# Performance work log

Measured on AMD Instinct MI355X. Metric: run time of the kernel, lower is better.

## Reference

```python
import jax, jax.numpy as jnp
import numpy as np

NF = 32      # feature channels
DG = 4       # deformable groups
K = 9        # 3x3 kernel taps


def _conv(x, w, b, stride=1):
    # x: [B,C,H,W], w: [O,I,3,3] (pad=1)
    y = jax.lax.conv_general_dilated(x, w, (stride, stride), ((1, 1), (1, 1)),
                                     dimension_numbers=('NCHW', 'OIHW', 'NCHW'))
    return y + b[None, :, None, None]


def _lrelu(x):
    return jnp.where(x >= 0, x, 0.1 * x)


def _up2(x):
    # bilinear, align_corners=False (half-pixel centers, matches torch F.interpolate)
    B, C, H, W = x.shape
    return jax.image.resize(x, (B, C, 2 * H, 2 * W), method='bilinear')


def _deform_conv(x, om, w, b):
    # Modulated deformable conv (DCNv2), stride=1, pad=1, dilation=1, 3x3.
    # x: [B,C,H,W]; om: [B,3*DG*K,H,W] = (offset_y | offset_x | mask) blocks.
    B, C, H, W = x.shape
    Cg = C // DG
    o1, o2, m = jnp.split(om, 3, axis=1)
    off_y = o1.reshape(B, DG, K, H, W)
    off_x = o2.reshape(B, DG, K, H, W)
    mask = jax.nn.sigmoid(m).reshape(B, DG, K, H, W)
    k = jnp.arange(K)
    dy = (k // 3 - 1).astype(x.dtype)            # kernel tap y displacement
    dx = (k % 3 - 1).astype(x.dtype)
    # sampling positions [B,DG,K,H,W]
    py = off_y + jnp.arange(H, dtype=x.dtype)[:, None] + dy[:, None, None]
    px = off_x + jnp.arange(W, dtype=x.dtype)[None, :] + dx[:, None, None]
    y0 = jnp.floor(py)
    x0 = jnp.floor(px)
    wy1 = py - y0
    wx1 = px - x0
    y0i = y0.astype(jnp.int32)
    x0i = x0.astype(jnp.int32)
    imgf = x.reshape(B, DG, Cg, H * W)

    def corner(yi, xi, wt):
        valid = (yi >= 0) & (yi < H) & (xi >= 0) & (xi < W)
        yc = jnp.clip(yi, 0, H - 1)
        xc = jnp.clip(xi, 0, W - 1)
        idx = (yc * W + xc).reshape(B, DG, 1, K * H * W)
        v = jnp.take_along_axis(imgf, idx, axis=3).reshape(B, DG, Cg, K, H, W)
        return v * (wt * valid)[:, :, None]

    samp = (corner(y0i, x0i, (1 - wy1) * (1 - wx1))
            + corner(y0i, x0i + 1, (1 - wy1) * wx1)
            + corner(y0i + 1, x0i, wy1 * (1 - wx1))
            + corner(y0i + 1, x0i + 1, wy1 * wx1))
    samp = samp * mask[:, :, None]                       # [B,DG,Cg,K,H,W]
    out = jnp.einsum('bgckhw,ogck->bohw', samp, w.reshape(w.shape[0], DG, Cg, K))
    return out + b[None, :, None, None]


_PARAM_SHAPES = [
    ('w1_1', (32, 64, 3, 3)), ('b1_1', (32,)),
    ('w2_1', (32, 32, 3, 3)), ('b2_1', (32,)),
    ('w3_1', (32, 32, 3, 3)), ('b3_1', (32,)),
    ('w4_1', (32, 32, 3, 3)), ('b4_1', (32,)),
    ('w6_1', (32, 32, 3, 3)), ('b6_1', (32,)),
    ('w7_1', (32, 32, 3, 3)), ('b7_1', (32,)),
    ('w1_2', (32, 64, 3, 3)), ('b1_2', (32,)),
    ('w2_2', (32, 32, 3, 3)), ('b2_2', (32,)),
    ('w3_2', (32, 64, 3, 3)), ('b3_2', (32,)),
    ('w4_2', (32, 32, 3, 3)), ('b4_2', (32,)),
    ('w_om', (108, 32, 3, 3)), ('b_om', (108,)),   # DCN_sep conv_offset_mask: 3*DG*K=108
    ('w_dcn', (32, 32, 3, 3)), ('b_dcn', (32,)),
]


def setup_inputs() -> dict:
    key = jax.random.key(0)
    ks = jax.random.split(key, len(_PARAM_SHAPES) + 2)
    B, H, W = 4, 192, 192
    d = {
        'fea1': jax.random.normal(ks[0], (B, NF, H, W), jnp.float32),
        'fea2': jax.random.normal(ks[1], (B, NF, H, W), jnp.float32),
    }
    for i, (name, shp) in enumerate(_PARAM_SHAPES):
        d[name] = jax.random.normal(ks[i + 2], shp, jnp.float32) * 0.05
    return d


def reference(fea1, fea2, w1_1, b1_1, w2_1, b2_1, w3_1, b3_1, w4_1, b4_1,
              w6_1, b6_1, w7_1, b7_1, w1_2, b1_2, w2_2, b2_2, w3_2, b3_2,
              w4_2, b4_2, w_om, b_om, w_dcn, b_dcn):
    off = _lrelu(_conv(jnp.concatenate([fea1, fea2], 1), w1_1, b1_1))
    off1 = _lrelu(_conv(off, w2_1, b2_1))
    off2 = _lrelu(_conv(off1, w3_1, b3_1, 2))   # H/2
    off2 = _lrelu(_conv(off2, w4_1, b4_1))
    off3 = _lrelu(_conv(off2, w6_1, b6_1, 2))   # H/4
    off3 = _lrelu(_conv(off3, w7_1, b7_1))
    up = _up2(off3)                              # back to H/2
    off = _lrelu(_conv(jnp.concatenate([up, off2], 1), w1_2, b1_2))
    off = _lrelu(_conv(off, w2_2, b2_2))
    up = _up2(off)                               # back to H
    off = _lrelu(_conv(jnp.concatenate([up, off1], 1), w3_2, b3_2))
    base_offset = _conv(off, w4_2, b4_2)
    om = _conv(base_offset, w_om, b_om)          # DCN_sep offset/mask head
    return _deform_conv(fea2, om, w_dcn, b_dcn)
```

## Files before the change

kernel.cpp:

```cpp
#include <hip/hip_runtime.h>
#include <math.h>


#define BDIM 256

typedef __attribute__((ext_vector_type(8))) short short8v;
typedef __attribute__((ext_vector_type(4))) float f32x4;

__device__ __forceinline__ unsigned short f2bf(float f) {
    unsigned u = __builtin_bit_cast(unsigned, f);
    u = (u + 0x7FFF + ((u >> 16) & 1)) >> 16;
    return (unsigned short)u;
}
__device__ __forceinline__ float bf2f(unsigned short h) {
    unsigned u = ((unsigned)h) << 16;
    return __builtin_bit_cast(float, u);
}

template<int NPASS, int NHALF, int NT, int STRIDE, bool LRELU>
__global__ __launch_bounds__(BDIM, 2)
void convm_k(const short* __restrict__ in0, const short* __restrict__ in1,
             const short* __restrict__ wf,
             const float* __restrict__ bias,
             short* __restrict__ out,
             int Hin, int Win, int Hout, int Wout, int OCS, int coutTot)
{
    const int lane = threadIdx.x & 63;
    const int wid  = blockIdx.x * 4 + (threadIdx.x >> 6);
    const int segs = Wout / (16 * NT);
    const int b  = wid / (Hout * segs);
    int r = wid - b * (Hout * segs);
    const int oy = r / segs;
    const int x0 = (r - oy * segs) * (16 * NT);
    const int lp = lane & 15;
    const int g  = lane >> 4;

    f32x4 acc[NT][NHALF];
#pragma unroll
    for (int nt = 0; nt < NT; ++nt)
#pragma unroll
        for (int h = 0; h < NHALF; ++h)
            acc[nt][h] = (f32x4){0.f, 0.f, 0.f, 0.f};

    const size_t inPlane = (size_t)Hin * Win * 32;
    const short8v zero = {};
    constexpr bool CACHE_A = (NHALF <= 2) && (NT > 1);

#pragma unroll
    for (int pass = 0; pass < NPASS; ++pass) {
        const short* inp = (pass == 0 ? in0 : in1) + (size_t)b * inPlane;

        short8v awc[CACHE_A ? 9 * NHALF : 1];
        if constexpr (CACHE_A) {
#pragma unroll
            for (int t = 0; t < 9; ++t)
#pragma unroll
                for (int h = 0; h < NHALF; ++h)
                    awc[t * NHALF + h] = *(const short8v*)(
                        wf + ((((size_t)pass * 9 + t) * NHALF + h) * 64 + lane) * 8);
        }

#pragma unroll
        for (int t = 0; t < 9; ++t) {
            const int iy = oy * STRIDE + t / 3 - 1;
            const bool rowok = (unsigned)iy < (unsigned)Hin;
            const int iyc = min(max(iy, 0), Hin - 1);

            short8v bvs[NT];
#pragma unroll
            for (int nt = 0; nt < NT; ++nt) {
                const int ox = x0 + nt * 16 + lp;
                const int ix = ox * STRIDE + t % 3 - 1;
                const bool ok = rowok & ((unsigned)ix < (unsigned)Win);
                const int ixc = min(max(ix, 0), Win - 1);
                short8v bv = *(const short8v*)(inp + ((size_t)iyc * Win + ixc) * 32 + g * 8);
                bvs[nt] = ok ? bv : zero;
            }
#pragma unroll
            for (int h = 0; h < NHALF; ++h) {
                short8v av;
                if constexpr (CACHE_A)
                    av = awc[t * NHALF + h];
                else
                    av = *(const short8v*)(
                        wf + ((((size_t)pass * 9 + t) * NHALF + h) * 64 + lane) * 8);
#pragma unroll
                for (int nt = 0; nt < NT; ++nt)
                    acc[nt][h] = __builtin_amdgcn_mfma_f32_16x16x32_bf16(
                        av, bvs[nt], acc[nt][h], 0, 0, 0);
            }
        }
    }

    const size_t outBase = ((size_t)b * Hout + oy) * Wout;
#pragma unroll
    for (int nt = 0; nt < NT; ++nt) {
        const int p = x0 + nt * 16 + lp;
        short* op = out + (outBase + p) * OCS;
#pragma unroll
        for (int h = 0; h < NHALF; ++h) {
            ushort4 st;
#pragma unroll
            for (int j = 0; j < 4; ++j) {
                const int co = h * 16 + g * 4 + j;
                float v = acc[nt][h][j] + bias[min(co, coutTot - 1)];
                if (LRELU) v = (v >= 0.f) ? v : 0.1f * v;
                ((unsigned short*)&st)[j] = f2bf(v);
            }
            const int co0 = h * 16 + g * 4;
            if (co0 < coutTot)
                *(ushort4*)(op + co0) = st;
        }
    }
}

struct WPArgs {
    const float* src[11];
    int off[11];
    int npass[11], nhalf[11], O[11];
};

__global__ __launch_bounds__(BDIM)
void wprep_k(WPArgs a, short* __restrict__ wbase)
{
    const int z = blockIdx.z;
    const int n = a.npass[z] * 9 * a.nhalf[z] * 512;
    const int idx = blockIdx.x * BDIM + threadIdx.x;
    if (idx >= n) return;
    const int j = idx & 7;
    const int l = (idx >> 3) & 63;
    int r = idx >> 9;
    const int h = r % a.nhalf[z]; r /= a.nhalf[z];
    const int t = r % 9;
    const int pass = r / 9;
    const int I = a.npass[z] * 32;
    const int cout = h * 16 + (l & 15);
    const int cin  = pass * 32 + (l >> 4) * 8 + j;
    float v = (cout < a.O[z]) ? a.src[z][((size_t)cout * I + cin) * 9 + t] : 0.f;
    wbase[a.off[z] + idx] = (short)f2bf(v);
}

__global__ __launch_bounds__(BDIM)
void wdp_k(const float* __restrict__ w, short* __restrict__ dst)
{
    const int idx = blockIdx.x * BDIM + threadIdx.x;
    if (idx >= 9 * 2 * 64 * 8) return;
    const int j = idx & 7;
    const int l = (idx >> 3) & 63;
    const int h = (idx >> 9) & 1;
    const int k = idx >> 10;
    const int cout = h * 16 + (l & 15);
    const int cin  = (l >> 4) * 8 + j;
    dst[idx] = (short)f2bf(w[((size_t)cout * 32 + cin) * 9 + k]);
}

__global__ __launch_bounds__(BDIM)
void cvtnhwc_k(const float* __restrict__ s0, const float* __restrict__ s1,
               short* __restrict__ d0, short* __restrict__ d1, int H, int W)
{
    const float* s = blockIdx.z ? s1 : s0;
    short* d = blockIdx.z ? d1 : d0;
    const int idx = blockIdx.x * BDIM + threadIdx.x;
    if (idx >= 4 * 32 * H * W) return;
    const int c = idx & 31;
    int t = idx >> 5;
    const int x = t % W; t /= W;
    const int y = t % H;
    const int b = t / H;
    d[idx] = (short)f2bf(s[(((size_t)b * 32 + c) * H + y) * W + x]);
}

__global__ __launch_bounds__(BDIM)
void up2b_k(const short* __restrict__ in, short* __restrict__ out,
            int Hin, int Win)
{
    const int Hout = 2 * Hin, Wout = 2 * Win;
    const int idx = blockIdx.x * BDIM + threadIdx.x;
    if (idx >= 4 * Hout * Wout * 4) return;
    const int cg = idx & 3;
    int t = idx >> 2;
    const int x = t % Wout; t /= Wout;
    const int y = t % Hout;
    const int b = t / Hout;

    const float sy = (y + 0.5f) * 0.5f - 0.5f;
    const float sx = (x + 0.5f) * 0.5f - 0.5f;
    const float y0f = floorf(sy), x0f = floorf(sx);
    const float wy = sy - y0f, wx = sx - x0f;
    const int y0 = (int)y0f, x0 = (int)x0f;
    const int y0c = min(max(y0, 0), Hin - 1);
    const int y1c = min(max(y0 + 1, 0), Hin - 1);
    const int x0c = min(max(x0, 0), Win - 1);
    const int x1c = min(max(x0 + 1, 0), Win - 1);

    const short* base = in + (size_t)b * Hin * Win * 32 + cg * 8;
    short8v v00 = *(const short8v*)(base + ((size_t)y0c * Win + x0c) * 32);
    short8v v01 = *(const short8v*)(base + ((size_t)y0c * Win + x1c) * 32);
    short8v v10 = *(const short8v*)(base + ((size_t)y1c * Win + x0c) * 32);
    short8v v11 = *(const short8v*)(base + ((size_t)y1c * Win + x1c) * 32);

    short8v o;
#pragma unroll
    for (int j = 0; j < 8; ++j) {
        float f = (1.f - wy) * ((1.f - wx) * bf2f((unsigned short)v00[j]) +
                                wx * bf2f((unsigned short)v01[j]))
                + wy * ((1.f - wx) * bf2f((unsigned short)v10[j]) +
                        wx * bf2f((unsigned short)v11[j]));
        o[j] = (short)f2bf(f);
    }
    short* op = out + (size_t)b * Hout * Wout * 32 + ((size_t)y * Wout + x) * 32 + cg * 8;
    *(short8v*)op = o;
}

__global__ __launch_bounds__(BDIM, 4)
void dcnm_k(const short* __restrict__ xb,
            const short* __restrict__ om,
            const short* __restrict__ wf,
            const float* __restrict__ bias,
            float* __restrict__ out, int H, int W)
{
    const int lane = threadIdx.x & 63;
    const int wid  = blockIdx.x * 4 + (threadIdx.x >> 6);
    const int segs = W / 16;
    const int b = wid / (H * segs);
    int r = wid - b * (H * segs);
    const int y = r / segs;
    const int x = (r - y * segs) * 16 + (lane & 15);
    const int g = lane >> 4;
    const size_t plane = (size_t)H * W;

    f32x4 acc0 = (f32x4){0.f, 0.f, 0.f, 0.f};
    f32x4 acc1 = (f32x4){0.f, 0.f, 0.f, 0.f};

    const short* omb = om + ((size_t)b * plane + (size_t)y * W + x) * 112;
    const short* xbb = xb + (size_t)b * plane * 32 + g * 8;

#pragma unroll
    for (int k = 0; k < 9; ++k) {
        const float offy = bf2f((unsigned short)omb[g * 9 + k]);
        const float offx = bf2f((unsigned short)omb[36 + g * 9 + k]);
        const float ml   = bf2f((unsigned short)omb[72 + g * 9 + k]);
        const float m = 1.f / (1.f + __expf(-ml));

        const float py = offy + (float)y + (float)(k / 3 - 1);
        const float px = offx + (float)x + (float)(k % 3 - 1);
        const float y0f = floorf(py), x0f = floorf(px);
        const int y0 = (int)y0f, x0 = (int)x0f;
        const float wy1 = py - y0f, wx1 = px - x0f;
        const float wy0 = 1.f - wy1, wx0 = 1.f - wx1;

        const bool y0ok = (unsigned)y0 < (unsigned)H;
        const bool y1ok = (unsigned)(y0 + 1) < (unsigned)H;
        const bool x0ok = (unsigned)x0 < (unsigned)W;
        const bool x1ok = (unsigned)(x0 + 1) < (unsigned)W;
        const int y0c = min(max(y0, 0), H - 1);
        const int y1c = min(max(y0 + 1, 0), H - 1);
        const int x0c = min(max(x0, 0), W - 1);
        const int x1c = min(max(x0 + 1, 0), W - 1);

        const float w00 = wy0 * wx0 * ((y0ok && x0ok) ? 1.f : 0.f) * m;
        const float w01 = wy0 * wx1 * ((y0ok && x1ok) ? 1.f : 0.f) * m;
        const float w10 = wy1 * wx0 * ((y1ok && x0ok) ? 1.f : 0.f) * m;
        const float w11 = wy1 * wx1 * ((y1ok && x1ok) ? 1.f : 0.f) * m;

        short8v v00 = *(const short8v*)(xbb + ((size_t)y0c * W + x0c) * 32);
        short8v v01 = *(const short8v*)(xbb + ((size_t)y0c * W + x1c) * 32);
        short8v v10 = *(const short8v*)(xbb + ((size_t)y1c * W + x0c) * 32);
        short8v v11 = *(const short8v*)(xbb + ((size_t)y1c * W + x1c) * 32);

        short8v bv;
#pragma unroll
        for (int j = 0; j < 8; ++j) {
            float s = w00 * bf2f((unsigned short)v00[j])
                    + w01 * bf2f((unsigned short)v01[j])
                    + w10 * bf2f((unsigned short)v10[j])
                    + w11 * bf2f((unsigned short)v11[j]);
            bv[j] = (short)f2bf(s);
        }

        short8v a0 = *(const short8v*)(wf + (((size_t)k * 2 + 0) * 64 + lane) * 8);
        short8v a1 = *(const short8v*)(wf + (((size_t)k * 2 + 1) * 64 + lane) * 8);
        acc0 = __builtin_amdgcn_mfma_f32_16x16x32_bf16(a0, bv, acc0, 0, 0, 0);
        acc1 = __builtin_amdgcn_mfma_f32_16x16x32_bf16(a1, bv, acc1, 0, 0, 0);
    }

    float* op = out + (size_t)b * 32 * plane + (size_t)y * W + x;
#pragma unroll
    for (int j = 0; j < 4; ++j) {
        const int co0 = g * 4 + j;
        const int co1 = 16 + g * 4 + j;
        op[(size_t)co0 * plane] = acc0[j] + bias[co0];
        op[(size_t)co1 * plane] = acc1[j] + bias[co1];
    }
}


extern "C" void kernel_launch(void* const* d_in, const int* in_sizes, int n_in,
                              void* d_out, int out_size, void* d_ws, size_t ws_size,
                              hipStream_t stream)
{
    const float* fea1  = (const float*)d_in[0];
    const float* fea2  = (const float*)d_in[1];
    const float* w1_1  = (const float*)d_in[2];  const float* b1_1 = (const float*)d_in[3];
    const float* w2_1  = (const float*)d_in[4];  const float* b2_1 = (const float*)d_in[5];
    const float* w3_1  = (const float*)d_in[6];  const float* b3_1 = (const float*)d_in[7];
    const float* w4_1  = (const float*)d_in[8];  const float* b4_1 = (const float*)d_in[9];
    const float* w6_1  = (const float*)d_in[10]; const float* b6_1 = (const float*)d_in[11];
    const float* w7_1  = (const float*)d_in[12]; const float* b7_1 = (const float*)d_in[13];
    const float* w1_2  = (const float*)d_in[14]; const float* b1_2 = (const float*)d_in[15];
    const float* w2_2  = (const float*)d_in[16]; const float* b2_2 = (const float*)d_in[17];
    const float* w3_2  = (const float*)d_in[18]; const float* b3_2 = (const float*)d_in[19];
    const float* w4_2  = (const float*)d_in[20]; const float* b4_2 = (const float*)d_in[21];
    const float* w_om  = (const float*)d_in[22]; const float* b_om = (const float*)d_in[23];
    const float* w_dcn = (const float*)d_in[24]; const float* b_dcn= (const float*)d_in[25];

    const int H = 192, W = 192;
    char* ws = (char*)d_ws;

    short* fea1b = (short*)(ws + 0);
    short* fea2b = (short*)(ws + 9437184);
    short* bufA  = (short*)(ws + 18874368);
    short* bufB  = (short*)(ws + 28311552);
    short* bufC  = (short*)(ws + 0);
    short* bufD  = (short*)(ws + 2359296);
    short* bufE  = (short*)(ws + 4718592);
    short* bufF  = (short*)(ws + 5308416);
    short* bufG  = (short*)(ws + 5898240);
    short* bufH  = (short*)(ws + 0);
    short* bufI  = (short*)(ws + 4718592);
    short* bufJ  = (short*)(ws + 37748736);
    short* bufK  = (short*)(ws + 18874368);
    short* bufL  = (short*)(ws + 0);
    short* om    = (short*)(ws + 37748736);
    short* wfrag = (short*)(ws + 70778880);
    short* wfdcn = (short*)(ws + 71083008);

    const int WOFF[11] = {0, 18432, 27648, 36864, 46080, 55296,
                          64512, 82944, 92160, 110592, 119808};

    dim3 blk(BDIM, 1, 1);

    {
        WPArgs a;
        const float* srcs[11] = {w1_1, w2_1, w3_1, w4_1, w6_1, w7_1,
                                 w1_2, w2_2, w3_2, w4_2, w_om};
        const int NP[11] = {2,1,1,1,1,1,2,1,2,1,1};
        const int NH[11] = {2,2,2,2,2,2,2,2,2,2,7};
        const int Os[11] = {32,32,32,32,32,32,32,32,32,32,108};
        for (int i = 0; i < 11; ++i) {
            a.src[i] = srcs[i]; a.off[i] = WOFF[i];
            a.npass[i] = NP[i]; a.nhalf[i] = NH[i]; a.O[i] = Os[i];
        }
        wprep_k<<<dim3(126, 1, 11), blk, 0, stream>>>(a, wfrag);
        cvtnhwc_k<<<dim3(18432, 1, 2), blk, 0, stream>>>(fea1, fea2, fea1b, fea2b, H, W);
        wdp_k<<<dim3(36), blk, 0, stream>>>(w_dcn, wfdcn);
    }

    convm_k<2,2,2,1,true><<<dim3(1152), blk, 0, stream>>>(
        fea1b, fea2b, wfrag + WOFF[0], b1_1, bufA, 192,192,192,192, 32, 32);
    convm_k<1,2,2,1,true><<<dim3(1152), blk, 0, stream>>>(
        bufA, nullptr, wfrag + WOFF[1], b2_1, bufB, 192,192,192,192, 32, 32);
    convm_k<1,2,1,2,true><<<dim3(576), blk, 0, stream>>>(
        bufB, nullptr, wfrag + WOFF[2], b3_1, bufC, 192,192,96,96, 32, 32);
    convm_k<1,2,1,1,true><<<dim3(576), blk, 0, stream>>>(
        bufC, nullptr, wfrag + WOFF[3], b4_1, bufD, 96,96,96,96, 32, 32);
    convm_k<1,2,1,2,true><<<dim3(144), blk, 0, stream>>>(
        bufD, nullptr, wfrag + WOFF[4], b6_1, bufE, 96,96,48,48, 32, 32);
    convm_k<1,2,1,1,true><<<dim3(144), blk, 0, stream>>>(
        bufE, nullptr, wfrag + WOFF[5], b7_1, bufF, 48,48,48,48, 32, 32);
    up2b_k<<<dim3(576), blk, 0, stream>>>(bufF, bufG, 48, 48);
    convm_k<2,2,1,1,true><<<dim3(576), blk, 0, stream>>>(
        bufG, bufD, wfrag + WOFF[6], b1_2, bufH, 96,96,96,96, 32, 32);
    convm_k<1,2,1,1,true><<<dim3(576), blk, 0, stream>>>(
        bufH, nullptr, wfrag + WOFF[7], b2_2, bufI, 96,96,96,96, 32, 32);
    up2b_k<<<dim3(2304), blk, 0, stream>>>(bufI, bufJ, 96, 96);
    convm_k<2,2,2,1,true><<<dim3(1152), blk, 0, stream>>>(
        bufJ, bufB, wfrag + WOFF[8], b3_2, bufK, 192,192,192,192, 32, 32);
    convm_k<1,2,2,1,false><<<dim3(1152), blk, 0, stream>>>(
        bufK, nullptr, wfrag + WOFF[9], b4_2, bufL, 192,192,192,192, 32, 32);
    convm_k<1,7,2,1,false><<<dim3(1152), blk, 0, stream>>>(
        bufL, nullptr, wfrag + WOFF[10], b_om, om, 192,192,192,192, 112, 108);
    dcnm_k<<<dim3(2304), blk, 0, stream>>>(
        fea2b, om, wfdcn, b_dcn, (float*)d_out, H, W);
}
```

Measured before the change: 334.1 us.

## Split om conv over output-channel grid, prefetch next tap input, raise occupancy

```diff
diff --git a/kernel.cpp b/kernel.cpp
--- a/kernel.cpp
+++ b/kernel.cpp
@@ -18,12 +18,13 @@
 }
 
 template<int NPASS, int NHALF, int NT, int STRIDE, bool LRELU>
-__global__ __launch_bounds__(BDIM, 2)
+__global__ __launch_bounds__(BDIM, 4)
 void convm_k(const short* __restrict__ in0, const short* __restrict__ in1,
              const short* __restrict__ wf,
              const float* __restrict__ bias,
              short* __restrict__ out,
-             int Hin, int Win, int Hout, int Wout, int OCS, int coutTot)
+             int Hin, int Win, int Hout, int Wout, int OCS, int coutTot,
+             int nhTot)
 {
     const int lane = threadIdx.x & 63;
     const int wid  = blockIdx.x * 4 + (threadIdx.x >> 6);
@@ -34,6 +35,25 @@
     const int x0 = (r - oy * segs) * (16 * NT);
     const int lp = lane & 15;
     const int g  = lane >> 4;
+    const int hBase = blockIdx.z * NHALF;
+    const int coutBase = blockIdx.z * NHALF * 16;
+
+    int rowOff[3]; bool rowOk[3];
+#pragma unroll
+    for (int ty = 0; ty < 3; ++ty) {
+        const int iy = oy * STRIDE + ty - 1;
+        rowOk[ty] = (unsigned)iy < (unsigned)Hin;
+        rowOff[ty] = min(max(iy, 0), Hin - 1) * Win;
+    }
+    int colOff[3][NT]; bool colOk[3][NT];
+#pragma unroll
+    for (int tx = 0; tx < 3; ++tx)
+#pragma unroll
+        for (int nt = 0; nt < NT; ++nt) {
+            const int ix = (x0 + nt * 16 + lp) * STRIDE + tx - 1;
+            colOk[tx][nt] = (unsigned)ix < (unsigned)Win;
+            colOff[tx][nt] = min(max(ix, 0), Win - 1) * 32 + g * 8;
+        }
 
     f32x4 acc[NT][NHALF];
 #pragma unroll
@@ -44,50 +64,41 @@
 
     const size_t inPlane = (size_t)Hin * Win * 32;
     const short8v zero = {};
-    constexpr bool CACHE_A = (NHALF <= 2) && (NT > 1);
 
 #pragma unroll
     for (int pass = 0; pass < NPASS; ++pass) {
         const short* inp = (pass == 0 ? in0 : in1) + (size_t)b * inPlane;
 
-        short8v awc[CACHE_A ? 9 * NHALF : 1];
-        if constexpr (CACHE_A) {
-#pragma unroll
-            for (int t = 0; t < 9; ++t)
-#pragma unroll
-                for (int h = 0; h < NHALF; ++h)
-                    awc[t * NHALF + h] = *(const short8v*)(
-                        wf + ((((size_t)pass * 9 + t) * NHALF + h) * 64 + lane) * 8);
+        short8v bcur[NT];
+#pragma unroll
+        for (int nt = 0; nt < NT; ++nt) {
+            short8v v = *(const short8v*)(inp + (size_t)rowOff[0] * 32 + colOff[0][nt]);
+            bcur[nt] = (rowOk[0] & colOk[0][nt]) ? v : zero;
         }
 
 #pragma unroll
         for (int t = 0; t < 9; ++t) {
-            const int iy = oy * STRIDE + t / 3 - 1;
-            const bool rowok = (unsigned)iy < (unsigned)Hin;
-            const int iyc = min(max(iy, 0), Hin - 1);
-
-            short8v bvs[NT];
-#pragma unroll
-            for (int nt = 0; nt < NT; ++nt) {
-                const int ox = x0 + nt * 16 + lp;
-                const int ix = ox * STRIDE + t % 3 - 1;
-                const bool ok = rowok & ((unsigned)ix < (unsigned)Win);
-                const int ixc = min(max(ix, 0), Win - 1);
-                short8v bv = *(const short8v*)(inp + ((size_t)iyc * Win + ixc) * 32 + g * 8);
-                bvs[nt] = ok ? bv : zero;
+            short8v bnxt[NT];
+            if (t < 8) {
+                const int ty = (t + 1) / 3, tx = (t + 1) % 3;
+#pragma unroll
+                for (int nt = 0; nt < NT; ++nt) {
+                    short8v v = *(const short8v*)(inp + (size_t)rowOff[ty] * 32 + colOff[tx][nt]);
+                    bnxt[nt] = (rowOk[ty] & colOk[tx][nt]) ? v : zero;
+                }
             }
 #pragma unroll
             for (int h = 0; h < NHALF; ++h) {
-                short8v av;
-                if constexpr (CACHE_A)
-                    av = awc[t * NHALF + h];
-                else
-                    av = *(const short8v*)(
-                        wf + ((((size_t)pass * 9 + t) * NHALF + h) * 64 + lane) * 8);
+                short8v av = *(const short8v*)(
+                    wf + ((((size_t)pass * 9 + t) * nhTot + hBase + h) * 64 + lane) * 8);
 #pragma unroll
                 for (int nt = 0; nt < NT; ++nt)
                     acc[nt][h] = __builtin_amdgcn_mfma_f32_16x16x32_bf16(
-                        av, bvs[nt], acc[nt][h], 0, 0, 0);
+                        av, bcur[nt], acc[nt][h], 0, 0, 0);
+            }
+            if (t < 8) {
+#pragma unroll
+                for (int nt = 0; nt < NT; ++nt) bcur[nt] = bnxt[nt];
             }
         }
     }
@@ -99,15 +110,14 @@
         short* op = out + (outBase + p) * OCS;
 #pragma unroll
         for (int h = 0; h < NHALF; ++h) {
+            const int co0 = coutBase + h * 16 + g * 4;
             ushort4 st;
 #pragma unroll
             for (int j = 0; j < 4; ++j) {
-                const int co = h * 16 + g * 4 + j;
-                float v = acc[nt][h][j] + bias[min(co, coutTot - 1)];
+                float v = acc[nt][h][j] + bias[min(co0 + j, coutTot - 1)];
                 if (LRELU) v = (v >= 0.f) ? v : 0.1f * v;
                 ((unsigned short*)&st)[j] = f2bf(v);
             }
-            const int co0 = h * 16 + g * 4;
             if (co0 < coutTot)
                 *(ushort4*)(op + co0) = st;
         }
@@ -333,7 +343,7 @@
     short* bufL  = (short*)(ws + 0);
     short* om    = (short*)(ws + 37748736);
     short* wfrag = (short*)(ws + 70778880);
-    short* wfdcn = (short*)(ws + 71083008);
+    short* wfdcn = (short*)(ws + 71092224);
 
     const int WOFF[11] = {0, 18432, 27648, 36864, 46080, 55296,
                           64512, 82944, 92160, 110592, 119808};
@@ -345,41 +355,41 @@
         const float* srcs[11] = {w1_1, w2_1, w3_1, w4_1, w6_1, w7_1,
                                  w1_2, w2_2, w3_2, w4_2, w_om};
         const int NP[11] = {2,1,1,1,1,1,2,1,2,1,1};
-        const int NH[11] = {2,2,2,2,2,2,2,2,2,2,7};
+        const int NH[11] = {2,2,2,2,2,2,2,2,2,2,8};
         const int Os[11] = {32,32,32,32,32,32,32,32,32,32,108};
         for (int i = 0; i < 11; ++i) {
             a.src[i] = srcs[i]; a.off[i] = WOFF[i];
             a.npass[i] = NP[i]; a.nhalf[i] = NH[i]; a.O[i] = Os[i];
         }
-        wprep_k<<<dim3(126, 1, 11), blk, 0, stream>>>(a, wfrag);
+        wprep_k<<<dim3(144, 1, 11), blk, 0, stream>>>(a, wfrag);
         cvtnhwc_k<<<dim3(18432, 1, 2), blk, 0, stream>>>(fea1, fea2, fea1b, fea2b, H, W);
         wdp_k<<<dim3(36), blk, 0, stream>>>(w_dcn, wfdcn);
     }
 
     convm_k<2,2,2,1,true><<<dim3(1152), blk, 0, stream>>>(
-        fea1b, fea2b, wfrag + WOFF[0], b1_1, bufA, 192,192,192,192, 32, 32);
+        fea1b, fea2b, wfrag + WOFF[0], b1_1, bufA, 192,192,192,192, 32, 32, 2);
     convm_k<1,2,2,1,true><<<dim3(1152), blk, 0, stream>>>(
-        bufA, nullptr, wfrag + WOFF[1], b2_1, bufB, 192,192,192,192, 32, 32);
+        bufA, nullptr, wfrag + WOFF[1], b2_1, bufB, 192,192,192,192, 32, 32, 2);
     convm_k<1,2,1,2,true><<<dim3(576), blk, 0, stream>>>(
-        bufB, nullptr, wfrag + WOFF[2], b3_1, bufC, 192,192,96,96, 32, 32);
+        bufB, nullptr, wfrag + WOFF[2], b3_1, bufC, 192,192,96,96, 32, 32, 2);
     convm_k<1,2,1,1,true><<<dim3(576), blk, 0, stream>>>(
-        bufC, nullptr, wfrag + WOFF[3], b4_1, bufD, 96,96,96,96, 32, 32);
+        bufC, nullptr, wfrag + WOFF[3], b4_1, bufD, 96,96,96,96, 32, 32, 2);
     convm_k<1,2,1,2,true><<<dim3(144), blk, 0, stream>>>(
-        bufD, nullptr, wfrag + WOFF[4], b6_1, bufE, 96,96,48,48, 32, 32);
+        bufD, nullptr, wfrag + WOFF[4], b6_1, bufE, 96,96,48,48, 32, 32, 2);
     convm_k<1,2,1,1,true><<<dim3(144), blk, 0, stream>>>(
-        bufE, nullptr, wfrag + WOFF[5], b7_1, bufF, 48,48,48,48, 32, 32);
+        bufE, nullptr, wfrag + WOFF[5], b7_1, bufF, 48,48,48,48, 32, 32, 2);
     up2b_k<<<dim3(576), blk, 0, stream>>>(bufF, bufG, 48, 48);
     convm_k<2,2,1,1,true><<<dim3(576), blk, 0, stream>>>(
-        bufG, bufD, wfrag + WOFF[6], b1_2, bufH, 96,96,96,96, 32, 32);
+        bufG, bufD, wfrag + WOFF[6], b1_2, bufH, 96,96,96,96, 32, 32, 2);
     convm_k<1,2,1,1,true><<<dim3(576), blk, 0, stream>>>(
-        bufH, nullptr, wfrag + WOFF[7], b2_2, bufI, 96,96,96,96, 32, 32);
+        bufH, nullptr, wfrag + WOFF[7], b2_2, bufI, 96,96,96,96, 32, 32, 2);
     up2b_k<<<dim3(2304), blk, 0, stream>>>(bufI, bufJ, 96, 96);
     convm_k<2,2,2,1,true><<<dim3(1152), blk, 0, stream>>>(
-        bufJ, bufB, wfrag + WOFF[8], b3_2, bufK, 192,192,192,192, 32, 32);
+        bufJ, bufB, wfrag + WOFF[8], b3_2, bufK, 192,192,192,192, 32, 32, 2);
     convm_k<1,2,2,1,false><<<dim3(1152), blk, 0, stream>>>(
-        bufK, nullptr, wfrag + WOFF[9], b4_2, bufL, 192,192,192,192, 32, 32);
-    convm_k<1,7,2,1,false><<<dim3(1152), blk, 0, stream>>>(
-        bufL, nullptr, wfrag + WOFF[10], b_om, om, 192,192,192,192, 112, 108);
+        bufK, nullptr, wfrag + WOFF[9], b4_2, bufL, 192,192,192,192, 32, 32, 2);
+    convm_k<1,2,2,1,false><<<dim3(1152, 1, 4), blk, 0, stream>>>(
+        bufL, nullptr, wfrag + WOFF[10], b_om, om, 192,192,192,192, 112, 108, 8);
     dcnm_k<<<dim3(2304), blk, 0, stream>>>(
         fea2b, om, wfdcn, b_dcn, (float*)d_out, H, W);
 }
```

Result: no change. 337.8 us (+1.1%).
